# Performance work log

Hardware: AMD Instinct MI355X
Metric: run time of the kernel (lower is better)

## Reference

```python
import jax, jax.numpy as jnp
import numpy as np


def setup_inputs() -> dict:
    key = jax.random.key(0)
    k1, k2, k3, k4 = jax.random.split(key, 4)
    B, V = 256, 128000
    logits = jax.random.normal(k1, (B, V), dtype=jnp.float32) * 4.0
    # temperatures in (0.5, 1.5); set a few rows to exactly 0 to exercise greedy path
    temperatures = jax.random.uniform(k2, (B,), dtype=jnp.float32, minval=0.5, maxval=1.5)
    temperatures = temperatures.at[:8].set(0.0)
    # top_ks in [0, 100); 0 means 'no top-k for this row'
    top_ks = jax.random.randint(k3, (B,), 0, 100, dtype=jnp.int32)
    # exponential(1) noise, matching torch.empty_like(probs).exponential_(1)
    exp_noise = jax.random.exponential(k4, (B, V), dtype=jnp.float32)
    return {"logits": logits, "temperatures": temperatures, "top_ks": top_ks,
            "exp_noise": exp_noise}


def reference(logits, temperatures, top_ks, exp_noise):
    logits = logits.astype(jnp.float32)            # [B, V]
    B, V = logits.shape
    greedy_tokens = jnp.argmax(logits, axis=-1)    # [B]

    # temperature scaling (rows with temp==0 take the greedy branch; avoid div-by-0)
    safe_temps = jnp.where(temperatures == 0, 1.0, temperatures)
    scaled = logits / safe_temps[:, None]          # [B, V]

    # vectorized per-row top-k threshold: sort descending, pick k-th value
    sorted_desc = jnp.sort(scaled, axis=-1)[:, ::-1]                     # [B, V]
    k_idx = jnp.clip(top_ks.astype(jnp.int32), 1, V) - 1                 # [B]
    threshold = jnp.take_along_axis(sorted_desc, k_idx[:, None], axis=1) # [B, 1]
    apply_topk = (top_ks > 0)[:, None]                                   # [B, 1]
    masked = jnp.where(apply_topk & (scaled < threshold), -jnp.inf, scaled)

    probs = jax.nn.softmax(masked, axis=-1)        # [B, V]

    # gumbel-max style sampling: argmax(probs / Exp(1))
    sample_tokens = jnp.argmax(probs / exp_noise, axis=-1)  # [B]

    return jnp.where(temperatures == 0, greedy_tokens, sample_tokens)
```

## Files before the change

### kernel.cpp

```cpp
#include <hip/hip_runtime.h>
#include <hip/hip_bf16.h>
#include <climits>
#include <cfloat>


#define V_SIZE 128000
#define NV4 (V_SIZE / 4)
#define BLOCK 1024
#define NWAVES (BLOCK / 64)
#define CAP 4096
#define ZCAP 64
#define BOUND 10.0f

__device__ __forceinline__ unsigned fkey(float f) {
    unsigned b = __float_as_uint(f);
    return (b & 0x80000000u) ? ~b : (b | 0x80000000u);
}
__device__ __forceinline__ float fkey_inv(unsigned k) {
    unsigned b = (k & 0x80000000u) ? (k & 0x7fffffffu) : ~k;
    return __uint_as_float(b);
}

__device__ __forceinline__ void amax_upd(float& v, int& i, float nv, int ni) {
    if (nv > v || (nv == v && ni < i)) { v = nv; i = ni; }
}

__device__ __forceinline__ void block_argmax(float& v, int& i, float* s_rv, int* s_ri) {
    const int tid = threadIdx.x, lane = tid & 63, wv = tid >> 6;
    __syncthreads();
#pragma unroll
    for (int off = 32; off > 0; off >>= 1) {
        float ov = __shfl_xor(v, off);
        int oi = __shfl_xor(i, off);
        amax_upd(v, i, ov, oi);
    }
    if (lane == 0) { s_rv[wv] = v; s_ri[wv] = i; }
    __syncthreads();
    if (tid < 64) {
        float vv = (lane < NWAVES) ? s_rv[lane] : -INFINITY;
        int ii = (lane < NWAVES) ? s_ri[lane] : INT_MAX;
#pragma unroll
        for (int off = 8; off > 0; off >>= 1) {
            float ov = __shfl_xor(vv, off);
            int oi = __shfl_xor(ii, off);
            amax_upd(vv, ii, ov, oi);
        }
        if (lane == 0) { s_rv[0] = vv; s_ri[0] = ii; }
    }
    __syncthreads();
    v = s_rv[0]; i = s_ri[0];
}

extern "C" __global__ void __launch_bounds__(BLOCK)
sampler_kernel(const float* __restrict__ logits, const float* __restrict__ temps,
               const int* __restrict__ topks, const float* __restrict__ noise,
               int* __restrict__ out) {
    const int row = blockIdx.x;
    const int tid = threadIdx.x;
    const float temp = temps[row];
    const int topk = topks[row];
    const float* __restrict__ lg = logits + (size_t)row * V_SIZE;
    const float* __restrict__ nz = noise + (size_t)row * V_SIZE;
    const float4* __restrict__ lg4 = reinterpret_cast<const float4*>(lg);
    const float4* __restrict__ nz4 = reinterpret_cast<const float4*>(nz);

    __shared__ float s_cval[CAP];
    __shared__ int s_cidx[CAP];
    __shared__ int s_zidx[ZCAP];
    __shared__ int s_ccount, s_zcount, s_nan, s_cnt;
    __shared__ float s_rv[NWAVES];
    __shared__ int s_ri[NWAVES];
    __shared__ float s_kth;

    const bool needTopk = (temp != 0.0f) && (topk > 0);

    if (tid == 0) { s_ccount = 0; s_zcount = 0; s_nan = INT_MAX; s_kth = -INFINITY; }
    __syncthreads();

    float bmax = -INFINITY; int bidx = INT_MAX;
    for (int b = tid; b < NV4; b += BLOCK) {
        float4 lv = lg4[b];
        float l[4] = {lv.x, lv.y, lv.z, lv.w};
        const int i0 = b << 2;
#pragma unroll
        for (int c = 0; c < 4; ++c) {
            amax_upd(bmax, bidx, l[c], i0 + c);
            if (needTopk && l[c] > BOUND) {
                int p = atomicAdd(&s_ccount, 1);
                if (p < CAP) { s_cval[p] = l[c]; s_cidx[p] = i0 + c; }
            }
        }
        if (needTopk) {
            float4 nv = nz4[b];
            float nn[4] = {nv.x, nv.y, nv.z, nv.w};
#pragma unroll
            for (int c = 0; c < 4; ++c) {
                if (nn[c] == 0.0f) {
                    int p = atomicAdd(&s_zcount, 1);
                    if (p < ZCAP) s_zidx[p] = i0 + c;
                }
            }
        }
    }
    __syncthreads();

    float gv = bmax; int gi = bidx;
    block_argmax(gv, gi, s_rv, s_ri);
    const int greedy = gi;

    if (temp == 0.0f) {
        if (tid == 0) out[row] = greedy;
        return;
    }

    int result;
    if (needTopk) {
        const int k = min(max(topk, 1), V_SIZE);
        const int n = s_ccount;
        float kthv = -INFINITY;
        bool cands_ok = (n <= CAP) && (n >= k);
        if (cands_ok) {
            for (int t = tid; t < n; t += BLOCK) {
                float v = s_cval[t];
                int g = 0, e = 0;
                for (int j = 0; j < n; ++j) {
                    float w = s_cval[j];
                    g += (w > v) ? 1 : 0;
                    e += (w == v) ? 1 : 0;
                }
                if (g < k && g + e >= k) s_kth = v;
            }
            __syncthreads();
            kthv = s_kth;
            if (!(kthv > BOUND + 0.5f)) cands_ok = false;
        }
        if (!cands_ok) {
            unsigned prefix = 0u;
            for (int bit = 31; bit >= 0; --bit) {
                const unsigned T = prefix | (1u << bit);
                if (tid == 0) s_cnt = 0;
                __syncthreads();
                int local = 0;
                for (int b = tid; b < NV4; b += BLOCK) {
                    float4 lv = lg4[b];
                    local += (fkey(lv.x) >= T);
                    local += (fkey(lv.y) >= T);
                    local += (fkey(lv.z) >= T);
                    local += (fkey(lv.w) >= T);
                }
#pragma unroll
                for (int off = 32; off > 0; off >>= 1) local += __shfl_xor(local, off);
                if ((tid & 63) == 0) atomicAdd(&s_cnt, local);
                __syncthreads();
                const int cnt = s_cnt;
                __syncthreads();
                if (cnt >= k) prefix = T;
            }
            kthv = fkey_inv(prefix);
        }
        const float thr = kthv / temp;

        const int zn = min(s_zcount, ZCAP);
        for (int t = tid; t < zn; t += BLOCK) {
            const int z = s_zidx[t];
            const float sc = lg[z] / temp;
            if (sc < thr) atomicMin(&s_nan, z);
        }

        float gb = -INFINITY; int gbi = INT_MAX;
        if (cands_ok) {
            for (int t = tid; t < n; t += BLOCK) {
                const float sc = s_cval[t] / temp;
                if (sc >= thr) {
                    const int ix = s_cidx[t];
                    const float g = sc - logf(nz[ix]);
                    amax_upd(gb, gbi, g, ix);
                }
            }
        } else {
            for (int b = tid; b < NV4; b += BLOCK) {
                float4 lv = lg4[b];
                float4 nv = nz4[b];
                float l[4] = {lv.x, lv.y, lv.z, lv.w};
                float nn[4] = {nv.x, nv.y, nv.z, nv.w};
                const int i0 = b << 2;
#pragma unroll
                for (int c = 0; c < 4; ++c) {
                    const float sc = l[c] / temp;
                    if (sc >= thr) {
                        const float g = sc - logf(nn[c]);
                        amax_upd(gb, gbi, g, i0 + c);
                    }
                }
            }
        }
        block_argmax(gb, gbi, s_rv, s_ri);
        result = (s_nan != INT_MAX) ? s_nan : gbi;
    } else {
        float gb = -INFINITY; int gbi = INT_MAX;
        for (int b = tid; b < NV4; b += BLOCK) {
            float4 lv = lg4[b];
            float4 nv = nz4[b];
            float l[4] = {lv.x, lv.y, lv.z, lv.w};
            float nn[4] = {nv.x, nv.y, nv.z, nv.w};
            const int i0 = b << 2;
#pragma unroll
            for (int c = 0; c < 4; ++c) {
                const float sc = l[c] / temp;
                const float g = sc - logf(nn[c]);
                amax_upd(gb, gbi, g, i0 + c);
            }
        }
        block_argmax(gb, gbi, s_rv, s_ri);
        result = gbi;
    }
    if (tid == 0) out[row] = result;
}

extern "C" void kernel_launch(void* const* d_in, const int* in_sizes, int n_in,
                              void* d_out, int out_size, void* d_ws, size_t ws_size,
                              hipStream_t stream) {
    const float* logits = (const float*)d_in[0];
    const float* temps  = (const float*)d_in[1];
    const int*   topks  = (const int*)d_in[2];
    const float* noise  = (const float*)d_in[3];
    int* out = (int*)d_out;
    const int B = in_sizes[1];
    sampler_kernel<<<B, BLOCK, 0, stream>>>(logits, temps, topks, noise, out);
}
```

Baseline: 83.03 us.

## Split greedy path and drop unused argmax from sampling rows

Greedy rows (temp==0) now run a dedicated argmax pass over the logits and return early. Sampling rows no longer compute the greedy argmax at all. The top-k candidate and zero-noise scans are split into separate passes, unrolled four loads deep, with a cheap max/min test per float4 before any per-element atomics. This cuts ALU work and branching in the first pass. The cost is that the noise row is now streamed in its own loop rather than interleaved with the logits loop.

```diff
diff --git a/kernel.cpp b/kernel.cpp
--- a/kernel.cpp
+++ b/kernel.cpp
@@ -49,6 +49,46 @@
     }
     __syncthreads();
     v = s_rv[0]; i = s_ri[0];
+}
+
+__device__ __forceinline__ void amax4(float4 v, int b, float& bmax, int& bidx) {
+    const float m = fmaxf(fmaxf(v.x, v.y), fmaxf(v.z, v.w));
+    if (m > bmax) {
+        const int i0 = b << 2;
+        bmax = m;
+        bidx = (v.x == m) ? i0 : (v.y == m) ? i0 + 1 : (v.z == m) ? i0 + 2 : i0 + 3;
+    }
+}
+
+__device__ __forceinline__ void cand4(float4 v, int b, float* s_cval, int* s_cidx,
+                                      int* s_ccount) {
+    const float m = fmaxf(fmaxf(v.x, v.y), fmaxf(v.z, v.w));
+    if (m > BOUND) {
+        const int i0 = b << 2;
+        const float l[4] = {v.x, v.y, v.z, v.w};
+#pragma unroll
+        for (int c = 0; c < 4; ++c) {
+            if (l[c] > BOUND) {
+                int p = atomicAdd(s_ccount, 1);
+                if (p < CAP) { s_cval[p] = l[c]; s_cidx[p] = i0 + c; }
+            }
+        }
+    }
+}
+
+__device__ __forceinline__ void zero4(float4 v, int b, int* s_zidx, int* s_zcount) {
+    const float mn = fminf(fminf(v.x, v.y), fminf(v.z, v.w));
+    if (mn == 0.0f) {
+        const int i0 = b << 2;
+        const float l[4] = {v.x, v.y, v.z, v.w};
+#pragma unroll
+        for (int c = 0; c < 4; ++c) {
+            if (l[c] == 0.0f) {
+                int p = atomicAdd(s_zcount, 1);
+                if (p < ZCAP) s_zidx[p] = i0 + c;
+            }
+        }
+    }
 }
 
 extern "C" __global__ void __launch_bounds__(BLOCK)
@@ -72,49 +112,57 @@
     __shared__ int s_ri[NWAVES];
     __shared__ float s_kth;
 
-    const bool needTopk = (temp != 0.0f) && (topk > 0);
+    if (temp == 0.0f) {
+        float bmax = -INFINITY; int bidx = INT_MAX;
+        int b = tid;
+        for (; b + 3 * BLOCK < NV4; b += 4 * BLOCK) {
+            float4 a0 = lg4[b];
+            float4 a1 = lg4[b + BLOCK];
+            float4 a2 = lg4[b + 2 * BLOCK];
+            float4 a3 = lg4[b + 3 * BLOCK];
+            amax4(a0, b, bmax, bidx);
+            amax4(a1, b + BLOCK, bmax, bidx);
+            amax4(a2, b + 2 * BLOCK, bmax, bidx);
+            amax4(a3, b + 3 * BLOCK, bmax, bidx);
+        }
+        for (; b < NV4; b += BLOCK) amax4(lg4[b], b, bmax, bidx);
+        block_argmax(bmax, bidx, s_rv, s_ri);
+        if (tid == 0) out[row] = bidx;
+        return;
+    }
 
     if (tid == 0) { s_ccount = 0; s_zcount = 0; s_nan = INT_MAX; s_kth = -INFINITY; }
     __syncthreads();
 
-    float bmax = -INFINITY; int bidx = INT_MAX;
-    for (int b = tid; b < NV4; b += BLOCK) {
-        float4 lv = lg4[b];
-        float l[4] = {lv.x, lv.y, lv.z, lv.w};
-        const int i0 = b << 2;
-#pragma unroll
-        for (int c = 0; c < 4; ++c) {
-            amax_upd(bmax, bidx, l[c], i0 + c);
-            if (needTopk && l[c] > BOUND) {
-                int p = atomicAdd(&s_ccount, 1);
-                if (p < CAP) { s_cval[p] = l[c]; s_cidx[p] = i0 + c; }
-            }
-        }
-        if (needTopk) {
-            float4 nv = nz4[b];
-            float nn[4] = {nv.x, nv.y, nv.z, nv.w};
-#pragma unroll
-            for (int c = 0; c < 4; ++c) {
-                if (nn[c] == 0.0f) {
-                    int p = atomicAdd(&s_zcount, 1);
-                    if (p < ZCAP) s_zidx[p] = i0 + c;
-                }
-            }
-        }
-    }
-    __syncthreads();
-
-    float gv = bmax; int gi = bidx;
-    block_argmax(gv, gi, s_rv, s_ri);
-    const int greedy = gi;
-
-    if (temp == 0.0f) {
-        if (tid == 0) out[row] = greedy;
-        return;
-    }
-
     int result;
-    if (needTopk) {
+    if (topk > 0) {
+        int b = tid;
+        for (; b + 3 * BLOCK < NV4; b += 4 * BLOCK) {
+            float4 a0 = lg4[b];
+            float4 a1 = lg4[b + BLOCK];
+            float4 a2 = lg4[b + 2 * BLOCK];
+            float4 a3 = lg4[b + 3 * BLOCK];
+            cand4(a0, b, s_cval, s_cidx, &s_ccount);
+            cand4(a1, b + BLOCK, s_cval, s_cidx, &s_ccount);
+            cand4(a2, b + 2 * BLOCK, s_cval, s_cidx, &s_ccount);
+            cand4(a3, b + 3 * BLOCK, s_cval, s_cidx, &s_ccount);
+        }
+        for (; b < NV4; b += BLOCK) cand4(lg4[b], b, s_cval, s_cidx, &s_ccount);
+
+        b = tid;
+        for (; b + 3 * BLOCK < NV4; b += 4 * BLOCK) {
+            float4 a0 = nz4[b];
+            float4 a1 = nz4[b + BLOCK];
+            float4 a2 = nz4[b + 2 * BLOCK];
+            float4 a3 = nz4[b + 3 * BLOCK];
+            zero4(a0, b, s_zidx, &s_zcount);
+            zero4(a1, b + BLOCK, s_zidx, &s_zcount);
+            zero4(a2, b + 2 * BLOCK, s_zidx, &s_zcount);
+            zero4(a3, b + 3 * BLOCK, s_zidx, &s_zcount);
+        }
+        for (; b < NV4; b += BLOCK) zero4(nz4[b], b, s_zidx, &s_zcount);
+        __syncthreads();
+
         const int k = min(max(topk, 1), V_SIZE);
         const int n = s_ccount;
         float kthv = -INFINITY;
@@ -141,8 +189,8 @@
                 if (tid == 0) s_cnt = 0;
                 __syncthreads();
                 int local = 0;
-                for (int b = tid; b < NV4; b += BLOCK) {
-                    float4 lv = lg4[b];
+                for (int q = tid; q < NV4; q += BLOCK) {
+                    float4 lv = lg4[q];
                     local += (fkey(lv.x) >= T);
                     local += (fkey(lv.y) >= T);
                     local += (fkey(lv.z) >= T);
@@ -178,12 +226,12 @@
                 }
             }
         } else {
-            for (int b = tid; b < NV4; b += BLOCK) {
-                float4 lv = lg4[b];
-                float4 nv = nz4[b];
-                float l[4] = {lv.x, lv.y, lv.z, lv.w};
-                float nn[4] = {nv.x, nv.y, nv.z, nv.w};
-                const int i0 = b << 2;
+            for (int q = tid; q < NV4; q += BLOCK) {
+                float4 lv = lg4[q];
+                float4 nv = nz4[q];
+                const float l[4] = {lv.x, lv.y, lv.z, lv.w};
+                const float nn[4] = {nv.x, nv.y, nv.z, nv.w};
+                const int i0 = q << 2;
 #pragma unroll
                 for (int c = 0; c < 4; ++c) {
                     const float sc = l[c] / temp;
@@ -198,12 +246,12 @@
         result = (s_nan != INT_MAX) ? s_nan : gbi;
     } else {
         float gb = -INFINITY; int gbi = INT_MAX;
-        for (int b = tid; b < NV4; b += BLOCK) {
-            float4 lv = lg4[b];
-            float4 nv = nz4[b];
-            float l[4] = {lv.x, lv.y, lv.z, lv.w};
-            float nn[4] = {nv.x, nv.y, nv.z, nv.w};
-            const int i0 = b << 2;
+        for (int q = tid; q < NV4; q += BLOCK) {
+            float4 lv = lg4[q];
+            float4 nv = nz4[q];
+            const float l[4] = {lv.x, lv.y, lv.z, lv.w};
+            const float nn[4] = {nv.x, nv.y, nv.z, nv.w};
+            const int i0 = q << 2;
 #pragma unroll
             for (int c = 0; c < 4; ++c) {
                 const float sc = l[c] / temp;
```

Result: faster. 70.64 us (-14.9%).
